# Kernel tuning notes

Hardware: AMD Instinct MI355X
Metric: run time of the kernel (lower is better)

The kernel has to match this reference:

```python
import jax, jax.numpy as jnp
import numpy as np

EPS = 1e-12

def _sn(w, u):
    # spectral norm, num_svs=1, num_itrs=1, eval mode (power iteration is
    # under no_grad in the original, so sv is a constant w.r.t. autodiff)
    Wm = w.reshape(w.shape[0], -1)          # [out, in*kh*kw]
    v = u @ Wm                               # [1, in*kh*kw]
    v = v / jnp.maximum(jnp.linalg.norm(v), EPS)
    u2 = v @ Wm.T                            # [1, out]
    u2 = u2 / jnp.maximum(jnp.linalg.norm(u2), EPS)
    sv = jnp.squeeze(v @ Wm.T @ u2.T)        # top singular value estimate
    return w / jax.lax.stop_gradient(sv)


def setup_inputs() -> dict:
    key = jax.random.key(0)
    ks = jax.random.split(key, 10)
    B, C, H, W = 32, 512, 64, 64
    Cr = C // 8
    return {
        'x':  jax.random.normal(ks[0], (B, C, H, W), jnp.float32),
        'w1': jax.random.normal(ks[1], (Cr, C, 1, 1), jnp.float32) * 0.05,
        'b1': jax.random.normal(ks[2], (Cr,), jnp.float32) * 0.02,
        'u1': jax.random.normal(ks[3], (1, Cr), jnp.float32),
        'w2': jax.random.normal(ks[4], (C, Cr, 1, 1), jnp.float32) * 0.05,
        'b2': jax.random.normal(ks[5], (C,), jnp.float32) * 0.02,
        'u2': jax.random.normal(ks[6], (1, C), jnp.float32),
        'w3': jax.random.normal(ks[7], (1, 2, 3, 3), jnp.float32) * 0.1,
        'b3': jax.random.normal(ks[8], (1,), jnp.float32) * 0.02,
        'u3': jax.random.normal(ks[9], (1, 1), jnp.float32),
    }


def reference(x, w1, b1, u1, w2, b2, u2, w3, b3, u3):
    # --- channel attention ---
    W1 = _sn(w1, u1).reshape(w1.shape[0], w1.shape[1])   # [Cr, C]
    W2 = _sn(w2, u2).reshape(w2.shape[0], w2.shape[1])   # [C, Cr]
    avg = jnp.mean(x, axis=(2, 3))                        # [B, C]
    mx  = jnp.max(x, axis=(2, 3))                         # [B, C]
    a = jax.nn.relu(avg @ W1.T + b1) @ W2.T + b2          # [B, C]
    m = jax.nn.relu(mx  @ W1.T + b1) @ W2.T + b2          # [B, C]
    s = jax.nn.sigmoid(a + m)
    x = x * s[:, :, None, None]
    # --- spatial attention ---
    ca = jnp.mean(x, axis=1, keepdims=True)               # [B,1,H,W]
    cm = jnp.max(x, axis=1, keepdims=True)                # [B,1,H,W]
    cat = jnp.concatenate([ca, cm], axis=1)               # [B,2,H,W]
    W3 = _sn(w3, u3)
    y = jax.lax.conv_general_dilated(
        cat, W3, window_strides=(1, 1), padding=((1, 1), (1, 1)),
        dimension_numbers=('NCHW', 'OIHW', 'NCHW'))
    y = y + b3.reshape(1, -1, 1, 1)
    return x * jax.nn.sigmoid(y)
```

## Files before the change

### kernel.cpp

```cpp
#include <hip/hip_runtime.h>


#define B_   32
#define C_   512
#define CR_  64
#define HW_  4096
#define WID_ 64
#define EPSF 1e-12f

__device__ __forceinline__ float sigmoidf(float x) {
  return 1.0f / (1.0f + __expf(-x));
}

__global__ __launch_bounds__(256) void pool_kernel(const float* __restrict__ x,
                                                   float* __restrict__ avg,
                                                   float* __restrict__ mx) {
  const int plane = blockIdx.x;
  const int t = threadIdx.x;
  const float4* xp = (const float4*)(x + (size_t)plane * HW_);
  float s = 0.0f, m = -INFINITY;
  #pragma unroll
  for (int q = 0; q < 4; q++) {
    float4 a = xp[q * 256 + t];
    s += (a.x + a.y) + (a.z + a.w);
    m = fmaxf(m, fmaxf(fmaxf(a.x, a.y), fmaxf(a.z, a.w)));
  }
  for (int o = 32; o > 0; o >>= 1) {
    s += __shfl_down(s, o);
    m = fmaxf(m, __shfl_down(m, o));
  }
  __shared__ float rs[4], rm[4];
  int wave = t >> 6, lane = t & 63;
  if (lane == 0) { rs[wave] = s; rm[wave] = m; }
  __syncthreads();
  if (t == 0) {
    float S = rs[0] + rs[1] + rs[2] + rs[3];
    float M = fmaxf(fmaxf(rm[0], rm[1]), fmaxf(rm[2], rm[3]));
    avg[plane] = S * (1.0f / HW_);
    mx[plane] = M;
  }
}

__device__ __forceinline__ float block_reduce_sum(float v, float* red) {
  int t = threadIdx.x;
  red[t] = v;
  __syncthreads();
  for (int o = 128; o > 0; o >>= 1) {
    if (t < o) red[t] += red[t + o];
    __syncthreads();
  }
  float r = red[0];
  __syncthreads();
  return r;
}

__global__ __launch_bounds__(256) void sv_kernel(const float* __restrict__ w1, const float* __restrict__ u1,
                                                 const float* __restrict__ w2, const float* __restrict__ u2,
                                                 const float* __restrict__ w3, const float* __restrict__ u3,
                                                 float* __restrict__ sv) {
  __shared__ float v[C_];
  __shared__ float red[256];
  const int t = threadIdx.x;

  for (int j = t; j < C_; j += 256) {
    float a = 0.0f;
    for (int i = 0; i < CR_; i++) a += u1[i] * w1[i * C_ + j];
    v[j] = a;
  }
  __syncthreads();
  float p = 0.0f;
  for (int j = t; j < C_; j += 256) p += v[j] * v[j];
  float nv = block_reduce_sum(p, red);
  float dv = fmaxf(sqrtf(nv), EPSF);
  float q = 0.0f;
  if (t < CR_) {
    float a = 0.0f;
    for (int j = 0; j < C_; j++) a += v[j] * w1[t * C_ + j];
    a /= dv;
    q = a * a;
  }
  float nt2 = block_reduce_sum(q, red);
  if (t == 0) sv[0] = nt2 / fmaxf(sqrtf(nt2), EPSF);
  __syncthreads();

  if (t < CR_) {
    float a = 0.0f;
    for (int i = 0; i < C_; i++) a += u2[i] * w2[i * CR_ + t];
    v[t] = a;
  }
  __syncthreads();
  p = (t < CR_) ? v[t] * v[t] : 0.0f;
  nv = block_reduce_sum(p, red);
  dv = fmaxf(sqrtf(nv), EPSF);
  q = 0.0f;
  for (int i = t; i < C_; i += 256) {
    float a = 0.0f;
    for (int j = 0; j < CR_; j++) a += v[j] * w2[i * CR_ + j];
    a /= dv;
    q += a * a;
  }
  nt2 = block_reduce_sum(q, red);
  if (t == 0) sv[1] = nt2 / fmaxf(sqrtf(nt2), EPSF);

  if (t == 0) {
    float u3v = u3[0];
    float nvs = 0.0f;
    for (int k = 0; k < 18; k++) { float vv = u3v * w3[k]; nvs += vv * vv; }
    float d = fmaxf(sqrtf(nvs), EPSF);
    float tt = 0.0f;
    for (int k = 0; k < 18; k++) tt += (u3v * w3[k] / d) * w3[k];
    float u2n = tt / fmaxf(fabsf(tt), EPSF);
    sv[2] = tt * u2n;
  }
}

__global__ __launch_bounds__(256) void mlp_kernel(const float* __restrict__ avg, const float* __restrict__ mx,
                                                  const float* __restrict__ w1, const float* __restrict__ b1,
                                                  const float* __restrict__ w2, const float* __restrict__ b2,
                                                  const float* __restrict__ sv, float* __restrict__ s) {
  const int b = blockIdx.x;
  const int t = threadIdx.x;
  __shared__ float pool[2][C_];
  __shared__ float hid[2][CR_];
  for (int i = t; i < C_; i += 256) {
    pool[0][i] = avg[b * C_ + i];
    pool[1][i] = mx[b * C_ + i];
  }
  __syncthreads();
  const float inv1 = 1.0f / sv[0];
  const float inv2 = 1.0f / sv[1];
  if (t < 2 * CR_) {
    int kind = t >> 6;
    int i = t & 63;
    const float4* wr = (const float4*)(w1 + (size_t)i * C_);
    float acc = 0.0f;
    for (int qq = 0; qq < C_ / 4; qq++) {
      float4 u = wr[qq];
      acc += pool[kind][qq * 4 + 0] * u.x + pool[kind][qq * 4 + 1] * u.y +
             pool[kind][qq * 4 + 2] * u.z + pool[kind][qq * 4 + 3] * u.w;
    }
    hid[kind][i] = fmaxf(acc * inv1 + b1[i], 0.0f);
  }
  __syncthreads();
  for (int c = t; c < C_; c += 256) {
    const float* wr = w2 + (size_t)c * CR_;
    float aa = 0.0f, mm = 0.0f;
    #pragma unroll 8
    for (int i = 0; i < CR_; i++) {
      float wv = wr[i];
      aa += hid[0][i] * wv;
      mm += hid[1][i] * wv;
    }
    float val = (aa + mm) * inv2 + 2.0f * b2[c];
    s[b * C_ + c] = sigmoidf(val);
  }
}

__global__ __launch_bounds__(256) void scale_pool_kernel(const float* __restrict__ x,
                                                         const float* __restrict__ s,
                                                         float* __restrict__ ca,
                                                         float* __restrict__ cm) {
  const int b = blockIdx.y;
  const int hw0 = blockIdx.x * 512;
  const int t = threadIdx.x;
  __shared__ float srow[C_];
  for (int i = t; i < C_; i += 256) srow[i] = s[b * C_ + i];
  __syncthreads();
  const int px = hw0 + t * 2;
  const float* xb = x + (size_t)b * C_ * HW_ + px;
  float s0 = 0.f, s1 = 0.f, m0 = -INFINITY, m1 = -INFINITY;
  #pragma unroll 8
  for (int c = 0; c < C_; c++) {
    float2 u = *(const float2*)(xb + (size_t)c * HW_);
    float sc = srow[c];
    float v0 = u.x * sc, v1 = u.y * sc;
    s0 += v0; s1 += v1;
    m0 = fmaxf(m0, v0); m1 = fmaxf(m1, v1);
  }
  *(float2*)(ca + b * HW_ + px) = make_float2(s0 * (1.0f / C_), s1 * (1.0f / C_));
  *(float2*)(cm + b * HW_ + px) = make_float2(m0, m1);
}

__global__ __launch_bounds__(256) void conv_out_kernel(const float* __restrict__ x,
                                                       const float* __restrict__ s,
                                                       const float* __restrict__ ca,
                                                       const float* __restrict__ cm,
                                                       const float* __restrict__ w3,
                                                       const float* __restrict__ b3,
                                                       const float* __restrict__ sv,
                                                       float* __restrict__ out) {
  const int b = blockIdx.y;
  const int hw0 = blockIdx.x * 512;
  const int t = threadIdx.x;
  __shared__ float srow[C_];
  for (int i = t; i < C_; i += 256) srow[i] = s[b * C_ + i];
  __syncthreads();
  const float inv3 = 1.0f / sv[2];
  float wn[18];
  #pragma unroll
  for (int k = 0; k < 18; k++) wn[k] = w3[k] * inv3;
  const float b3f = b3[0];

  float sy[2];
  #pragma unroll
  for (int e = 0; e < 2; e++) {
    int px = hw0 + t * 2 + e;
    int h = px >> 6, w = px & 63;
    float acc = b3f;
    #pragma unroll
    for (int dh = -1; dh <= 1; dh++) {
      int hh = h + dh;
      if (hh < 0 || hh >= 64) continue;
      #pragma unroll
      for (int dw = -1; dw <= 1; dw++) {
        int ww = w + dw;
        if (ww < 0 || ww >= WID_) continue;
        int n = b * HW_ + hh * WID_ + ww;
        int k = (dh + 1) * 3 + (dw + 1);
        acc += ca[n] * wn[k] + cm[n] * wn[9 + k];
      }
    }
    sy[e] = sigmoidf(acc);
  }

  const int px = hw0 + t * 2;
  const float* xb = x + (size_t)b * C_ * HW_ + px;
  float* ob = out + (size_t)b * C_ * HW_ + px;
  #pragma unroll 8
  for (int c = 0; c < C_; c++) {
    float2 u = *(const float2*)(xb + (size_t)c * HW_);
    float sc = srow[c];
    *(float2*)(ob + (size_t)c * HW_) = make_float2(u.x * sc * sy[0], u.y * sc * sy[1]);
  }
}

extern "C" void kernel_launch(void* const* d_in, const int* in_sizes, int n_in,
                              void* d_out, int out_size, void* d_ws, size_t ws_size,
                              hipStream_t stream) {
  const float* x  = (const float*)d_in[0];
  const float* w1 = (const float*)d_in[1];
  const float* b1 = (const float*)d_in[2];
  const float* u1 = (const float*)d_in[3];
  const float* w2 = (const float*)d_in[4];
  const float* b2 = (const float*)d_in[5];
  const float* u2 = (const float*)d_in[6];
  const float* w3 = (const float*)d_in[7];
  const float* b3 = (const float*)d_in[8];
  const float* u3 = (const float*)d_in[9];

  float* ws = (float*)d_ws;
  float* avg = ws;
  float* mx  = ws + 16384;
  float* s   = ws + 32768;
  float* sv  = ws + 49152;
  float* ca  = ws + 65536;
  float* cm  = ws + 196608;

  pool_kernel<<<B_ * C_, 256, 0, stream>>>(x, avg, mx);
  sv_kernel<<<1, 256, 0, stream>>>(w1, u1, w2, u2, w3, u3, sv);
  mlp_kernel<<<B_, 256, 0, stream>>>(avg, mx, w1, b1, w2, b2, sv, s);
  scale_pool_kernel<<<dim3(8, B_), 256, 0, stream>>>(x, s, ca, cm);
  conv_out_kernel<<<dim3(8, B_), 256, 0, stream>>>(x, s, ca, cm, w3, b3, sv, (float*)d_out);
}
```

Measured before the change: 689.4 us.

## Split spectral-norm work across blocks, widen channel pooling, and stream output separately

The single-block spectral-norm kernel becomes three blocks, one per weight, each with vectorized loads and parallel dot products. The scale-and-pool kernel now uses 1024 threads that split channels four ways and combine partial sums and maxes through shared memory. The fused conv-plus-output kernel is split into a small conv kernel that writes the spatial gate to workspace and a grid-stride float4 elementwise output kernel. The main aim is to replace the original 256-block launches, which use few compute units and have long serial per-thread channel loops, with launches that expose more parallelism for the bandwidth-bound passes. The cost is an extra launch and a round trip of the spatial gate through memory.

```diff
diff --git a/kernel.cpp b/kernel.cpp
--- a/kernel.cpp
+++ b/kernel.cpp
@@ -60,57 +60,82 @@
                                                  float* __restrict__ sv) {
   __shared__ float v[C_];
   __shared__ float red[256];
-  const int t = threadIdx.x;
-
-  for (int j = t; j < C_; j += 256) {
+  __shared__ float tmp[C_];
+  const int t = threadIdx.x;
+  const int blk = blockIdx.x;
+
+  if (blk == 0) {
+    if (t < CR_) tmp[t] = u1[t];
+    __syncthreads();
+    float ax = 0.0f, ay = 0.0f;
+    for (int i = 0; i < CR_; i++) {
+      float ui = tmp[i];
+      float2 wv = *(const float2*)(w1 + (size_t)i * C_ + 2 * t);
+      ax += ui * wv.x; ay += ui * wv.y;
+    }
+    v[2 * t] = ax; v[2 * t + 1] = ay;
+    float nv = block_reduce_sum(ax * ax + ay * ay, red);
+    float dv = fmaxf(sqrtf(nv), EPSF);
+    int i = t >> 2, part = t & 3;
+    const float4* wr = (const float4*)(w1 + (size_t)i * C_ + part * 128);
+    float acc = 0.0f;
+    #pragma unroll 8
+    for (int q = 0; q < 32; q++) {
+      float4 wv = wr[q];
+      int j = part * 128 + 4 * q;
+      acc += v[j] * wv.x + v[j + 1] * wv.y + v[j + 2] * wv.z + v[j + 3] * wv.w;
+    }
+    acc += __shfl_down(acc, 2);
+    acc += __shfl_down(acc, 1);
+    float q2 = 0.0f;
+    if (part == 0) { float a2 = acc / dv; q2 = a2 * a2; }
+    float nt2 = block_reduce_sum(q2, red);
+    if (t == 0) sv[0] = nt2 / fmaxf(sqrtf(nt2), EPSF);
+
+  } else if (blk == 1) {
+    for (int i = t; i < C_; i += 256) tmp[i] = u2[i];
+    __syncthreads();
+    int j = t & 63, ig = t >> 6;
+    const float* wp = w2 + (size_t)ig * 128 * CR_ + j;
     float a = 0.0f;
-    for (int i = 0; i < CR_; i++) a += u1[i] * w1[i * C_ + j];
-    v[j] = a;
-  }
-  __syncthreads();
-  float p = 0.0f;
-  for (int j = t; j < C_; j += 256) p += v[j] * v[j];
-  float nv = block_reduce_sum(p, red);
-  float dv = fmaxf(sqrtf(nv), EPSF);
-  float q = 0.0f;
-  if (t < CR_) {
-    float a = 0.0f;
-    for (int j = 0; j < C_; j++) a += v[j] * w1[t * C_ + j];
-    a /= dv;
-    q = a * a;
-  }
-  float nt2 = block_reduce_sum(q, red);
-  if (t == 0) sv[0] = nt2 / fmaxf(sqrtf(nt2), EPSF);
-  __syncthreads();
-
-  if (t < CR_) {
-    float a = 0.0f;
-    for (int i = 0; i < C_; i++) a += u2[i] * w2[i * CR_ + t];
-    v[t] = a;
-  }
-  __syncthreads();
-  p = (t < CR_) ? v[t] * v[t] : 0.0f;
-  nv = block_reduce_sum(p, red);
-  dv = fmaxf(sqrtf(nv), EPSF);
-  q = 0.0f;
-  for (int i = t; i < C_; i += 256) {
-    float a = 0.0f;
-    for (int j = 0; j < CR_; j++) a += v[j] * w2[i * CR_ + j];
-    a /= dv;
-    q += a * a;
-  }
-  nt2 = block_reduce_sum(q, red);
-  if (t == 0) sv[1] = nt2 / fmaxf(sqrtf(nt2), EPSF);
-
-  if (t == 0) {
-    float u3v = u3[0];
-    float nvs = 0.0f;
-    for (int k = 0; k < 18; k++) { float vv = u3v * w3[k]; nvs += vv * vv; }
-    float d = fmaxf(sqrtf(nvs), EPSF);
-    float tt = 0.0f;
-    for (int k = 0; k < 18; k++) tt += (u3v * w3[k] / d) * w3[k];
-    float u2n = tt / fmaxf(fabsf(tt), EPSF);
-    sv[2] = tt * u2n;
+    #pragma unroll 8
+    for (int i = 0; i < 128; i++) a += tmp[ig * 128 + i] * wp[(size_t)i * CR_];
+    red[t] = a;
+    __syncthreads();
+    if (t < CR_) v[t] = red[t] + red[t + 64] + red[t + 128] + red[t + 192];
+    __syncthreads();
+    float p = (t < CR_) ? v[t] * v[t] : 0.0f;
+    float nv = block_reduce_sum(p, red);
+    float dv = fmaxf(sqrtf(nv), EPSF);
+    float q = 0.0f;
+    #pragma unroll
+    for (int rep = 0; rep < 2; rep++) {
+      int i = t + rep * 256;
+      const float4* wr = (const float4*)(w2 + (size_t)i * CR_);
+      float acc = 0.0f;
+      #pragma unroll
+      for (int qq = 0; qq < 16; qq++) {
+        float4 wv = wr[qq];
+        acc += v[4 * qq] * wv.x + v[4 * qq + 1] * wv.y +
+               v[4 * qq + 2] * wv.z + v[4 * qq + 3] * wv.w;
+      }
+      acc /= dv;
+      q += acc * acc;
+    }
+    float nt2 = block_reduce_sum(q, red);
+    if (t == 0) sv[1] = nt2 / fmaxf(sqrtf(nt2), EPSF);
+
+  } else {
+    if (t == 0) {
+      float u3v = u3[0];
+      float nvs = 0.0f;
+      for (int k = 0; k < 18; k++) { float vv = u3v * w3[k]; nvs += vv * vv; }
+      float d = fmaxf(sqrtf(nvs), EPSF);
+      float tt = 0.0f;
+      for (int k = 0; k < 18; k++) tt += (u3v * w3[k] / d) * w3[k];
+      float u2n = tt / fmaxf(fabsf(tt), EPSF);
+      sv[2] = tt * u2n;
+    }
   }
 }
 
@@ -156,52 +181,59 @@
   }
 }
 
-__global__ __launch_bounds__(256) void scale_pool_kernel(const float* __restrict__ x,
-                                                         const float* __restrict__ s,
-                                                         float* __restrict__ ca,
-                                                         float* __restrict__ cm) {
+__global__ __launch_bounds__(1024) void scale_pool_kernel(const float* __restrict__ x,
+                                                          const float* __restrict__ s,
+                                                          float* __restrict__ ca,
+                                                          float* __restrict__ cm) {
   const int b = blockIdx.y;
   const int hw0 = blockIdx.x * 512;
   const int t = threadIdx.x;
+  const int pxid = t & 255;
+  const int cg = t >> 8;
   __shared__ float srow[C_];
-  for (int i = t; i < C_; i += 256) srow[i] = s[b * C_ + i];
-  __syncthreads();
-  const int px = hw0 + t * 2;
+  for (int i = t; i < C_; i += 1024) srow[i] = s[b * C_ + i];
+  __syncthreads();
+  const int px = hw0 + pxid * 2;
   const float* xb = x + (size_t)b * C_ * HW_ + px;
   float s0 = 0.f, s1 = 0.f, m0 = -INFINITY, m1 = -INFINITY;
+  const int c0 = cg * 128;
   #pragma unroll 8
-  for (int c = 0; c < C_; c++) {
+  for (int c = c0; c < c0 + 128; c++) {
     float2 u = *(const float2*)(xb + (size_t)c * HW_);
     float sc = srow[c];
     float v0 = u.x * sc, v1 = u.y * sc;
     s0 += v0; s1 += v1;
     m0 = fmaxf(m0, v0); m1 = fmaxf(m1, v1);
   }
-  *(float2*)(ca + b * HW_ + px) = make_float2(s0 * (1.0f / C_), s1 * (1.0f / C_));
-  *(float2*)(cm + b * HW_ + px) = make_float2(m0, m1);
-}
-
-__global__ __launch_bounds__(256) void conv_out_kernel(const float* __restrict__ x,
-                                                       const float* __restrict__ s,
-                                                       const float* __restrict__ ca,
-                                                       const float* __restrict__ cm,
-                                                       const float* __restrict__ w3,
-                                                       const float* __restrict__ b3,
-                                                       const float* __restrict__ sv,
-                                                       float* __restrict__ out) {
+  __shared__ float rs0[4][256], rs1[4][256], rm0[4][256], rm1[4][256];
+  rs0[cg][pxid] = s0; rs1[cg][pxid] = s1;
+  rm0[cg][pxid] = m0; rm1[cg][pxid] = m1;
+  __syncthreads();
+  if (cg == 0) {
+    float S0 = rs0[0][pxid] + rs0[1][pxid] + rs0[2][pxid] + rs0[3][pxid];
+    float S1 = rs1[0][pxid] + rs1[1][pxid] + rs1[2][pxid] + rs1[3][pxid];
+    float M0 = fmaxf(fmaxf(rm0[0][pxid], rm0[1][pxid]), fmaxf(rm0[2][pxid], rm0[3][pxid]));
+    float M1 = fmaxf(fmaxf(rm1[0][pxid], rm1[1][pxid]), fmaxf(rm1[2][pxid], rm1[3][pxid]));
+    *(float2*)(ca + (size_t)b * HW_ + px) = make_float2(S0 * (1.0f / C_), S1 * (1.0f / C_));
+    *(float2*)(cm + (size_t)b * HW_ + px) = make_float2(M0, M1);
+  }
+}
+
+__global__ __launch_bounds__(256) void conv_sy_kernel(const float* __restrict__ ca,
+                                                      const float* __restrict__ cm,
+                                                      const float* __restrict__ w3,
+                                                      const float* __restrict__ b3,
+                                                      const float* __restrict__ sv,
+                                                      float* __restrict__ sy) {
   const int b = blockIdx.y;
   const int hw0 = blockIdx.x * 512;
   const int t = threadIdx.x;
-  __shared__ float srow[C_];
-  for (int i = t; i < C_; i += 256) srow[i] = s[b * C_ + i];
-  __syncthreads();
   const float inv3 = 1.0f / sv[2];
   float wn[18];
   #pragma unroll
   for (int k = 0; k < 18; k++) wn[k] = w3[k] * inv3;
   const float b3f = b3[0];
 
-  float sy[2];
   #pragma unroll
   for (int e = 0; e < 2; e++) {
     int px = hw0 + t * 2 + e;
@@ -220,17 +252,30 @@
         acc += ca[n] * wn[k] + cm[n] * wn[9 + k];
       }
     }
-    sy[e] = sigmoidf(acc);
-  }
-
-  const int px = hw0 + t * 2;
-  const float* xb = x + (size_t)b * C_ * HW_ + px;
-  float* ob = out + (size_t)b * C_ * HW_ + px;
-  #pragma unroll 8
-  for (int c = 0; c < C_; c++) {
-    float2 u = *(const float2*)(xb + (size_t)c * HW_);
-    float sc = srow[c];
-    *(float2*)(ob + (size_t)c * HW_) = make_float2(u.x * sc * sy[0], u.y * sc * sy[1]);
+    sy[b * HW_ + px] = sigmoidf(acc);
+  }
+}
+
+__global__ __launch_bounds__(256) void out_kernel(const float* __restrict__ x,
+                                                  const float* __restrict__ s,
+                                                  const float* __restrict__ sy,
+                                                  float* __restrict__ out) {
+  const size_t N4 = (size_t)B_ * C_ * HW_ / 4;
+  const size_t stride = (size_t)gridDim.x * blockDim.x;
+  for (size_t i = (size_t)blockIdx.x * blockDim.x + threadIdx.x; i < N4; i += stride) {
+    size_t base = i * 4;
+    int hw = (int)(base & (HW_ - 1));
+    int bc = (int)(base >> 12);
+    int b  = bc >> 9;
+    float sc = s[bc];
+    float4 u = ((const float4*)x)[i];
+    float4 g = *(const float4*)(sy + (size_t)b * HW_ + hw);
+    float4 r;
+    r.x = u.x * sc * g.x;
+    r.y = u.y * sc * g.y;
+    r.z = u.z * sc * g.z;
+    r.w = u.w * sc * g.w;
+    ((float4*)out)[i] = r;
   }
 }
 
@@ -255,10 +300,12 @@
   float* sv  = ws + 49152;
   float* ca  = ws + 65536;
   float* cm  = ws + 196608;
+  float* sy  = ws + 327680;
 
   pool_kernel<<<B_ * C_, 256, 0, stream>>>(x, avg, mx);
-  sv_kernel<<<1, 256, 0, stream>>>(w1, u1, w2, u2, w3, u3, sv);
+  sv_kernel<<<3, 256, 0, stream>>>(w1, u1, w2, u2, w3, u3, sv);
   mlp_kernel<<<B_, 256, 0, stream>>>(avg, mx, w1, b1, w2, b2, sv, s);
-  scale_pool_kernel<<<dim3(8, B_), 256, 0, stream>>>(x, s, ca, cm);
-  conv_out_kernel<<<dim3(8, B_), 256, 0, stream>>>(x, s, ca, cm, w3, b3, sv, (float*)d_out);
-}
+  scale_pool_kernel<<<dim3(8, B_), 1024, 0, stream>>>(x, s, ca, cm);
+  conv_sy_kernel<<<dim3(8, B_), 256, 0, stream>>>(ca, cm, w3, b3, sv, sy);
+  out_kernel<<<2048, 256, 0, stream>>>(x, s, sy, (float*)d_out);
+}
```

Result: faster. 584.1 us (-15.3%).
